# Kernel optimization log

Hardware: AMD Instinct MI355X
Metric: run time of the kernel (lower is better)

## Reference

```python
import jax, jax.numpy as jnp
import numpy as np

HID = 2048      # hidden_size
H = 16          # num query heads
KV = 4          # num kv heads
HD = HID // H   # head_dim = 128
THETA = 1000000.0
T = 2048        # tokens (single causal sequence)


def _rope(x, positions):
    # neox-style rotate-half RoPE over full head_dim. x: [T, h, HD]
    half = HD // 2
    inv_freq = THETA ** (-jnp.arange(half, dtype=jnp.float32) * 2.0 / HD)  # [half]
    freqs = positions.astype(jnp.float32)[:, None] * inv_freq              # [T, half]
    cos = jnp.cos(freqs)[:, None, :]
    sin = jnp.sin(freqs)[:, None, :]
    x1, x2 = x[..., :half], x[..., half:]
    return jnp.concatenate([x1 * cos - x2 * sin, x2 * cos + x1 * sin], axis=-1)


def setup_inputs() -> dict:
    key = jax.random.key(0)
    k1, k2, k3 = jax.random.split(key, 3)
    hidden_states = jax.random.normal(k1, (T, HID), jnp.float32) * 0.02
    w_qkv = jax.random.normal(k2, (HID, (H + 2 * KV) * HD), jnp.float32) * 0.02
    w_o = jax.random.normal(k3, (H * HD, HID), jnp.float32) * 0.02
    positions = jnp.arange(T, dtype=jnp.int32)
    return {"hidden_states": hidden_states, "w_qkv": w_qkv, "w_o": w_o,
            "positions": positions}


def reference(hidden_states, w_qkv, w_o, positions):
    q_size, kv_size = H * HD, KV * HD
    qkv = hidden_states @ w_qkv                                  # [T, q+2kv]
    q = qkv[:, :q_size].reshape(T, H, HD)
    k = qkv[:, q_size:q_size + kv_size].reshape(T, KV, HD)
    v = qkv[:, q_size + kv_size:].reshape(T, KV, HD)
    q = _rope(q, positions)
    k = _rope(k, positions)
    # GQA: expand kv heads to query heads
    group = H // KV
    k_e = jnp.repeat(k, group, axis=1)                           # [T, H, HD]
    v_e = jnp.repeat(v, group, axis=1)
    scale = HD ** -0.5
    scores = jnp.einsum('thd,shd->hts', q, k_e) * scale          # [H, T, T]
    causal = positions[:, None] >= positions[None, :]            # [T, T]
    scores = jnp.where(causal[None, :, :], scores, -1e30)
    attn = jax.nn.softmax(scores, axis=-1)
    o = jnp.einsum('hts,shd->thd', attn, v_e).reshape(T, H * HD)
    return o @ w_o
```

## Files before the change

kernel.cpp:

```cpp
#include <hip/hip_runtime.h>
#include <hip/hip_bf16.h>

#define T_LEN 2048
#define HID 2048
#define NH 16
#define NKV 4
#define HD 128
#define QKV_COLS 3072

typedef __attribute__((ext_vector_type(8))) short bf16x8;
typedef __attribute__((ext_vector_type(4))) float f32x4;

static __device__ __forceinline__ ushort f2bf(float f) {
  __hip_bfloat16 h = __float2bfloat16(f);
  return *reinterpret_cast<ushort*>(&h);
}
static __device__ __forceinline__ float bf2f(ushort u) {
  union { unsigned int i; float f; } v;
  v.i = ((unsigned int)u) << 16;
  return v.f;
}

static __device__ __forceinline__ void async_copy16(const ushort* g, ushort* l) {
  __builtin_amdgcn_global_load_lds(
      (const __attribute__((address_space(1))) unsigned int*)g,
      (__attribute__((address_space(3))) unsigned int*)l, 16, 0, 0);
}

__global__ __launch_bounds__(256) void cast_f32_bf16(
    const float* __restrict__ x, ushort* __restrict__ y, int n) {
  int idx = (blockIdx.x * 256 + threadIdx.x) * 4;
  if (idx < n) {
    float4 v = *(const float4*)(x + idx);
    ushort4 o;
    o.x = f2bf(v.x); o.y = f2bf(v.y); o.z = f2bf(v.z); o.w = f2bf(v.w);
    *(ushort4*)(y + idx) = o;
  }
}

__global__ __launch_bounds__(256) void transpose_cast(
    const float* __restrict__ W, ushort* __restrict__ WT, int K, int N) {
  __shared__ float t[64][65];
  const int bk = blockIdx.x * 64, bn = blockIdx.y * 64;
  const int tid = threadIdx.x;
  const int c = tid & 63;
#pragma unroll
  for (int i = 0; i < 16; ++i) {
    int r = (tid >> 6) + i * 4;
    t[r][c] = W[(size_t)(bk + r) * N + bn + c];
  }
  __syncthreads();
#pragma unroll
  for (int i = 0; i < 16; ++i) {
    int r = (tid >> 6) + i * 4;
    WT[(size_t)(bn + r) * K + bk + c] = f2bf(t[c][r]);
  }
}

__global__ __launch_bounds__(64) void rope_table(
    float2* __restrict__ tbl, const int* __restrict__ positions) {
  const int t = blockIdx.x, j = threadIdx.x;
  double inv_freq = pow(1000000.0, -(double)(2 * j) / 128.0);
  double ang = (double)positions[t] * inv_freq;
  double s, c;
  sincos(ang, &s, &c);
  tbl[(size_t)t * 64 + j] = make_float2((float)c, (float)s);
}

template <bool OUT_BF16>
__global__ __launch_bounds__(256, 5) void gemm_bt(
    const ushort* __restrict__ A, const ushort* __restrict__ BT,
    void* __restrict__ C, int M, int N, int K) {
  __shared__ __align__(16) ushort lds[1536 * 8];
  const int tid = threadIdx.x;
  const int bm = blockIdx.y * 64, bn = blockIdx.x * 128;
  const int wave = tid >> 6, lane = tid & 63;
  const int lr = lane & 15, lq = lane >> 4;
  const int wm = (wave & 1) * 32, wn = (wave >> 1) * 64;

  f32x4 acc[2][4];
#pragma unroll
  for (int i = 0; i < 2; ++i)
#pragma unroll
    for (int j = 0; j < 4; ++j) {
      acc[i][j][0] = 0.f; acc[i][j][1] = 0.f;
      acc[i][j][2] = 0.f; acc[i][j][3] = 0.f;
    }

  for (int k0 = 0; k0 < K; k0 += 64) {
#pragma unroll
    for (int it = 0; it < 2; ++it) {
      int c = it * 256 + tid;
      int row = c >> 3, sl = c & 7, kc = sl ^ (row & 7);
      async_copy16(A + (size_t)(bm + row) * K + k0 + kc * 8, &lds[c * 8]);
    }
#pragma unroll
    for (int it = 0; it < 4; ++it) {
      int c = it * 256 + tid;
      int row = c >> 3, sl = c & 7, kc = sl ^ (row & 7);
      async_copy16(BT + (size_t)(bn + row) * K + k0 + kc * 8,
                   &lds[(512 + c) * 8]);
    }
    __syncthreads();

#pragma unroll
    for (int ks = 0; ks < 2; ++ks) {
      bf16x8 af[2], bfr[4];
#pragma unroll
      for (int mi = 0; mi < 2; ++mi) {
        int row = wm + mi * 16 + lr, kc = ks * 4 + lq;
        af[mi] = *(const bf16x8*)&lds[(row * 8 + (kc ^ (row & 7))) * 8];
      }
#pragma unroll
      for (int ni = 0; ni < 4; ++ni) {
        int row = wn + ni * 16 + lr, kc = ks * 4 + lq;
        bfr[ni] = *(const bf16x8*)&lds[(512 + row * 8 + (kc ^ (row & 7))) * 8];
      }
#pragma unroll
      for (int mi = 0; mi < 2; ++mi)
#pragma unroll
        for (int ni = 0; ni < 4; ++ni)
          acc[mi][ni] = __builtin_amdgcn_mfma_f32_16x16x32_bf16(
              af[mi], bfr[ni], acc[mi][ni], 0, 0, 0);
    }
    __syncthreads();
  }

#pragma unroll
  for (int mi = 0; mi < 2; ++mi)
#pragma unroll
    for (int ni = 0; ni < 4; ++ni)
#pragma unroll
      for (int r = 0; r < 4; ++r) {
        size_t row = bm + wm + mi * 16 + lq * 4 + r;
        size_t col = bn + wn + ni * 16 + lr;
        if (OUT_BF16)
          ((ushort*)C)[row * N + col] = f2bf(acc[mi][ni][r]);
        else
          ((float*)C)[row * N + col] = acc[mi][ni][r];
      }
}

__global__ __launch_bounds__(256, 5) void gemm_qkv(
    const ushort* __restrict__ A, const ushort* __restrict__ BT,
    ushort* __restrict__ qkvb, const float2* __restrict__ tbl,
    int M, int N, int K) {
  __shared__ __align__(16) ushort lds[1536 * 8];
  const int tid = threadIdx.x;
  const int bm = blockIdx.y * 64, bn = blockIdx.x * 128;
  const int wave = tid >> 6, lane = tid & 63;
  const int lr = lane & 15, lq = lane >> 4;
  const int wm = (wave & 1) * 32, wn = (wave >> 1) * 64;

  f32x4 acc[2][4];
#pragma unroll
  for (int i = 0; i < 2; ++i)
#pragma unroll
    for (int j = 0; j < 4; ++j) {
      acc[i][j][0] = 0.f; acc[i][j][1] = 0.f;
      acc[i][j][2] = 0.f; acc[i][j][3] = 0.f;
    }

  for (int k0 = 0; k0 < K; k0 += 64) {
#pragma unroll
    for (int it = 0; it < 2; ++it) {
      int c = it * 256 + tid;
      int row = c >> 3, sl = c & 7, kc = sl ^ (row & 7);
      async_copy16(A + (size_t)(bm + row) * K + k0 + kc * 8, &lds[c * 8]);
    }
#pragma unroll
    for (int it = 0; it < 4; ++it) {
      int c = it * 256 + tid;
      int row = c >> 3, sl = c & 7, kc = sl ^ (row & 7);
      async_copy16(BT + (size_t)(bn + row) * K + k0 + kc * 8,
                   &lds[(512 + c) * 8]);
    }
    __syncthreads();

#pragma unroll
    for (int ks = 0; ks < 2; ++ks) {
      bf16x8 af[2], bfr[4];
#pragma unroll
      for (int mi = 0; mi < 2; ++mi) {
        int row = wm + mi * 16 + lr, kc = ks * 4 + lq;
        af[mi] = *(const bf16x8*)&lds[(row * 8 + (kc ^ (row & 7))) * 8];
      }
#pragma unroll
      for (int ni = 0; ni < 4; ++ni) {
        int row = wn + ni * 16 + lr, kc = ks * 4 + lq;
        bfr[ni] = *(const bf16x8*)&lds[(512 + row * 8 + (kc ^ (row & 7))) * 8];
      }
#pragma unroll
      for (int mi = 0; mi < 2; ++mi)
#pragma unroll
        for (int ni = 0; ni < 4; ++ni)
          acc[mi][ni] = __builtin_amdgcn_mfma_f32_16x16x32_bf16(
              af[mi], bfr[ni], acc[mi][ni], 0, 0, 0);
    }
    __syncthreads();
  }

  const int head = bn >> 7;
  if (head < NH + NKV - NKV + 0 + (NKV) - 4 + 16 + 4 - 0 && head < 20) {
    ushort* ep = lds;
#pragma unroll
    for (int mi = 0; mi < 2; ++mi)
#pragma unroll
      for (int ni = 0; ni < 4; ++ni)
#pragma unroll
        for (int r = 0; r < 4; ++r)
          ep[(wm + mi * 16 + lq * 4 + r) * 130 + wn + ni * 16 + lr] =
              f2bf(acc[mi][ni][r]);
    __syncthreads();

    const float qs = (head < NH) ? 0.08838834764831845f : 1.0f;
#pragma unroll
    for (int it = 0; it < 16; ++it) {
      int idx = it * 256 + tid;
      int row = idx >> 6, j = idx & 63;
      float x1 = bf2f(ep[row * 130 + j]);
      float x2 = bf2f(ep[row * 130 + 64 + j]);
      float2 cs = tbl[(size_t)(bm + row) * 64 + j];
      qkvb[(size_t)(bm + row) * QKV_COLS + bn + j] =
          f2bf((x1 * cs.x - x2 * cs.y) * qs);
      qkvb[(size_t)(bm + row) * QKV_COLS + bn + 64 + j] =
          f2bf((x2 * cs.x + x1 * cs.y) * qs);
    }
  } else {
#pragma unroll
    for (int mi = 0; mi < 2; ++mi)
#pragma unroll
      for (int ni = 0; ni < 4; ++ni)
#pragma unroll
        for (int r = 0; r < 4; ++r) {
          size_t row = bm + wm + mi * 16 + lq * 4 + r;
          size_t col = bn + wn + ni * 16 + lr;
          qkvb[row * QKV_COLS + col] = f2bf(acc[mi][ni][r]);
        }
  }
}

__global__ __launch_bounds__(256) void repack_vt(
    const ushort* __restrict__ qkv, ushort* __restrict__ vt) {
  __shared__ ushort tile[64][65];
  const int bt = blockIdx.x * 64;
  const int bv = blockIdx.y * 64;
  const int tid = threadIdx.x;
  const int c = tid & 63, r0 = tid >> 6;
#pragma unroll
  for (int i = 0; i < 16; ++i) {
    int r = r0 + i * 4;
    tile[r][c] = qkv[(size_t)(bt + r) * QKV_COLS + 2560 + bv + c];
  }
  __syncthreads();
#pragma unroll
  for (int i = 0; i < 16; ++i) {
    int r = r0 + i * 4;
    vt[(size_t)(bv + r) * T_LEN + bt + c] = tile[c][r];
  }
}

__global__ __launch_bounds__(256, 3) void attn_mfma(
    const ushort* __restrict__ qkv, const ushort* __restrict__ vt,
    ushort* __restrict__ o, ushort* __restrict__ partials,
    float* __restrict__ ml) {
  int qt, h, k_begin, k_end, slot = -1;
  {
    const int i = blockIdx.x;
    if (i < 512) {
      qt = 31 - (i >> 5);
      const int rem = i & 31;
      h = rem >> 1;
      const int chunk = rem & 1;
      const int n = qt + 1, half = n >> 1;
      k_begin = chunk ? half : 0;
      k_end = chunk ? n : half;
      slot = ((qt - 16) * 16 + h) * 2 + chunk;
    } else {
      const int j = i - 512;
      qt = 15 - (j >> 4);
      h = j & 15;
      k_begin = 0;
      k_end = qt + 1;
    }
  }
  const int kh = h >> 2;
  const int tid = threadIdx.x;
  const int wave = tid >> 6, lane = tid & 63;
  const int lr = lane & 15, lq = lane >> 4;
  const int wq = wave >> 1, ws = wave & 1;

  __shared__ __align__(16) ushort KsL[1024 * 8];
  __shared__ __align__(16) ushort VtsL[1024 * 8];
  __shared__ __align__(16) ushort Ps[8 * 67 * 8];
  __shared__ float l_sh[64][2];

  bf16x8 qf[2][4];
  {
    const ushort* qbase =
        qkv + (size_t)(qt * 64 + wq * 32 + lr) * QKV_COLS + h * HD + lq * 8;
#pragma unroll
    for (int mi = 0; mi < 2; ++mi)
#pragma unroll
      for (int kk = 0; kk < 4; ++kk)
        qf[mi][kk] = *(const bf16x8*)(qbase + (size_t)mi * 16 * QKV_COLS + kk * 32);
  }

  float l_part[2][4];
#pragma unroll
  for (int mi = 0; mi < 2; ++mi)
#pragma unroll
    for (int r = 0; r < 4; ++r) l_part[mi][r] = 0.f;
  f32x4 o_acc[4][2];
#pragma unroll
  for (int qi = 0; qi < 4; ++qi)
#pragma unroll
    for (int di = 0; di < 2; ++di) {
      o_acc[qi][di][0] = 0.f; o_acc[qi][di][1] = 0.f;
      o_acc[qi][di][2] = 0.f; o_acc[qi][di][3] = 0.f;
    }

  for (int kt = k_begin; kt < k_end; ++kt) {
    __syncthreads();

    {
      const ushort* kbase = qkv + 2048 + kh * HD;
#pragma unroll
      for (int it = 0; it < 4; ++it) {
        int c = it * 256 + tid;
        int s = c >> 4, sl = c & 15, dg = sl ^ (s & 15);
        async_copy16(kbase + (size_t)(kt * 64 + s) * QKV_COLS + dg * 8,
                     &KsL[c * 8]);
      }
    }
    {
      const ushort* vbase = vt + (size_t)(kh * HD) * T_LEN + kt * 64;
#pragma unroll
      for (int it = 0; it < 4; ++it) {
        int c = it * 256 + tid;
        int d = c >> 3, sl = c & 7, sc = sl ^ (d & 7);
        async_copy16(vbase + (size_t)d * T_LEN + sc * 8, &VtsL[c * 8]);
      }
    }
    __syncthreads();

    f32x4 s_acc[2][2];
#pragma unroll
    for (int mi = 0; mi < 2; ++mi)
#pragma unroll
      for (int ni = 0; ni < 2; ++ni) {
        s_acc[mi][ni][0] = 0.f; s_acc[mi][ni][1] = 0.f;
        s_acc[mi][ni][2] = 0.f; s_acc[mi][ni][3] = 0.f;
      }
#pragma unroll
    for (int kk = 0; kk < 4; ++kk) {
      bf16x8 kf[2];
#pragma unroll
      for (int ni = 0; ni < 2; ++ni) {
        int s = ws * 32 + ni * 16 + lr;
        kf[ni] = *(const bf16x8*)&KsL[(s * 16 + ((kk * 4 + lq) ^ (s & 15))) * 8];
      }
#pragma unroll
      for (int mi = 0; mi < 2; ++mi)
#pragma unroll
        for (int ni = 0; ni < 2; ++ni)
          s_acc[mi][ni] = __builtin_amdgcn_mfma_f32_16x16x32_bf16(
              qf[mi][kk], kf[ni], s_acc[mi][ni], 0, 0, 0);
    }

    if (kt == qt) {
#pragma unroll
      for (int mi = 0; mi < 2; ++mi)
#pragma unroll
        for (int ni = 0; ni < 2; ++ni)
#pragma unroll
          for (int r = 0; r < 4; ++r)
            if (ws * 32 + ni * 16 + lr > wq * 32 + mi * 16 + lq * 4 + r)
              s_acc[mi][ni][r] = -1e30f;
    }

#pragma unroll
    for (int mi = 0; mi < 2; ++mi)
#pragma unroll
      for (int ni = 0; ni < 2; ++ni)
#pragma unroll
        for (int r = 0; r < 4; ++r) {
          float p = __expf(s_acc[mi][ni][r]);
          l_part[mi][r] += p;
          int s = ws * 32 + ni * 16 + lr;
          int q = wq * 32 + mi * 16 + lq * 4 + r;
          Ps[((s >> 3) * 67 + q) * 8 + (s & 7)] = f2bf(p);
        }
    __syncthreads();

#pragma unroll
    for (int ss = 0; ss < 2; ++ss) {
      bf16x8 vf[2];
#pragma unroll
      for (int di = 0; di < 2; ++di) {
        int d = wave * 32 + di * 16 + lr, sc = ss * 4 + lq;
        vf[di] = *(const bf16x8*)&VtsL[(d * 8 + (sc ^ (d & 7))) * 8];
      }
#pragma unroll
      for (int qi = 0; qi < 4; ++qi) {
        bf16x8 pf = *(const bf16x8*)&Ps[((ss * 4 + lq) * 67 + qi * 16 + lr) * 8];
#pragma unroll
        for (int di = 0; di < 2; ++di)
          o_acc[qi][di] = __builtin_amdgcn_mfma_f32_16x16x32_bf16(
              pf, vf[di], o_acc[qi][di], 0, 0, 0);
      }
    }
  }

#pragma unroll
  for (int mi = 0; mi < 2; ++mi)
#pragma unroll
    for (int r = 0; r < 4; ++r) {
      float v = l_part[mi][r];
#pragma unroll
      for (int off = 1; off < 16; off <<= 1) v += __shfl_xor(v, off, 16);
      l_part[mi][r] = v;
    }
  if (lr == 0) {
#pragma unroll
    for (int mi = 0; mi < 2; ++mi)
#pragma unroll
      for (int r = 0; r < 4; ++r)
        l_sh[wq * 32 + mi * 16 + lq * 4 + r][ws] = l_part[mi][r];
  }
  __syncthreads();

  if (slot < 0) {
    ushort* ob = o + (size_t)(qt * 64) * (NH * HD) + h * HD + wave * 32;
#pragma unroll
    for (int qi = 0; qi < 4; ++qi)
#pragma unroll
      for (int r = 0; r < 4; ++r) {
        int q = qi * 16 + lq * 4 + r;
        float inv = 1.f / (l_sh[q][0] + l_sh[q][1]);
#pragma unroll
        for (int di = 0; di < 2; ++di)
          ob[(size_t)q * (NH * HD) + di * 16 + lr] =
              f2bf(o_acc[qi][di][r] * inv);
      }
  } else {
    ushort* pb = partials + (size_t)slot * 64 * HD + wave * 32;
#pragma unroll
    for (int qi = 0; qi < 4; ++qi)
#pragma unroll
      for (int r = 0; r < 4; ++r) {
        int q = qi * 16 + lq * 4 + r;
#pragma unroll
        for (int di = 0; di < 2; ++di)
          pb[(size_t)q * HD + di * 16 + lr] = f2bf(o_acc[qi][di][r]);
      }
    if (tid < 64) ml[(size_t)slot * 64 + tid] = l_sh[tid][0] + l_sh[tid][1];
  }
}

__global__ __launch_bounds__(256) void attn_reduce(
    const ushort* __restrict__ partials, const float* __restrict__ ml,
    ushort* __restrict__ o) {
  const int bi = blockIdx.x;
  const int qt = 16 + (bi >> 4), h = bi & 15;
  const int s0 = ((qt - 16) * 16 + h) * 2;
  const int tid = threadIdx.x;
  const int row = tid >> 2;
  const int dq = (tid & 3) * 32;

  float l0 = ml[(size_t)s0 * 64 + row];
  float l1 = ml[(size_t)(s0 + 1) * 64 + row];
  float inv = 1.f / (l0 + l1);

  const ushort* p0 = partials + ((size_t)s0 * 64 + row) * HD + dq;
  const ushort* p1 = partials + ((size_t)(s0 + 1) * 64 + row) * HD + dq;
  ushort* ob = o + (size_t)(qt * 64 + row) * (NH * HD) + h * HD + dq;
#pragma unroll
  for (int k = 0; k < 32; ++k)
    ob[k] = f2bf((bf2f(p0[k]) + bf2f(p1[k])) * inv);
}

extern "C" void kernel_launch(void* const* d_in, const int* in_sizes, int n_in,
                              void* d_out, int out_size, void* d_ws,
                              size_t ws_size, hipStream_t stream) {
  const float* hidden = (const float*)d_in[0];
  const float* w_qkv  = (const float*)d_in[1];
  const float* w_o    = (const float*)d_in[2];
  const int* positions = (const int*)d_in[3];
  float* out = (float*)d_out;

  ushort* ws = (ushort*)d_ws;
  ushort* hb    = ws;
  ushort* wqkvT = ws + 4194304;
  ushort* qkvb  = wqkvT + 6291456;
  ushort* vtb   = qkvb + 6291456;
  float*  mlb   = (float*)(vtb + 1048576);
  float2* tbl   = (float2*)(mlb + 32768);
  ushort* ob       = hb;
  ushort* partials = wqkvT;
  ushort* woT      = wqkvT;

  cast_f32_bf16<<<4096, 256, 0, stream>>>(hidden, hb, HID * T_LEN);
  transpose_cast<<<dim3(HID / 64, QKV_COLS / 64), 256, 0, stream>>>(
      w_qkv, wqkvT, HID, QKV_COLS);
  rope_table<<<T_LEN, 64, 0, stream>>>(tbl, positions);

  gemm_qkv<<<dim3(QKV_COLS / 128, T_LEN / 64), 256, 0, stream>>>(
      hb, wqkvT, qkvb, tbl, T_LEN, QKV_COLS, HID);

  repack_vt<<<dim3(T_LEN / 64, (NKV * HD) / 64), 256, 0, stream>>>(qkvb, vtb);

  attn_mfma<<<768, 256, 0, stream>>>(qkvb, vtb, ob, partials, mlb);
  attn_reduce<<<256, 256, 0, stream>>>(partials, mlb, ob);

  transpose_cast<<<dim3(HID / 64, HID / 64), 256, 0, stream>>>(
      w_o, woT, HID, HID);

  gemm_bt<false><<<dim3(HID / 128, T_LEN / 64), 256, 0, stream>>>(
      ob, woT, out, T_LEN, HID, NH * HD);
}
```

Before: 212.4 us.

## Double-buffer GEMM LDS loads, fuse prep kernels, write V transpose in QKV epilogue

Merges the hidden cast, w_qkv transpose-cast and RoPE table into one prep launch. Both GEMMs now double-buffer their LDS tiles so the next K-slice is prefetched while MFMAs run on the current one. Occupancy hints drop from 5 to 3 blocks to fit the doubled LDS. The QKV GEMM epilogue writes the V columns straight into the transposed vt buffer, which removes the separate repack_vt kernel and its extra pass over V. The V path no longer writes V into qkvb, which assumes attention reads V only from vt.

```diff
diff --git a/kernel.cpp b/kernel.cpp
--- a/kernel.cpp
+++ b/kernel.cpp
@@ -27,14 +27,42 @@
       (__attribute__((address_space(3))) unsigned int*)l, 16, 0, 0);
 }
 
-__global__ __launch_bounds__(256) void cast_f32_bf16(
-    const float* __restrict__ x, ushort* __restrict__ y, int n) {
-  int idx = (blockIdx.x * 256 + threadIdx.x) * 4;
-  if (idx < n) {
-    float4 v = *(const float4*)(x + idx);
+__global__ __launch_bounds__(256) void prep(
+    const float* __restrict__ hidden, ushort* __restrict__ hb,
+    const float* __restrict__ w_qkv, ushort* __restrict__ wqkvT,
+    const int* __restrict__ positions, float2* __restrict__ tbl) {
+  __shared__ float t[64][65];
+  const int b = blockIdx.x;
+  const int tid = threadIdx.x;
+  if (b < 4096) {
+    int idx = (b * 256 + tid) * 4;
+    float4 v = *(const float4*)(hidden + idx);
     ushort4 o;
     o.x = f2bf(v.x); o.y = f2bf(v.y); o.z = f2bf(v.z); o.w = f2bf(v.w);
-    *(ushort4*)(y + idx) = o;
+    *(ushort4*)(hb + idx) = o;
+  } else if (b < 5632) {
+    const int tb = b - 4096;
+    const int bk = (tb & 31) * 64, bn = (tb >> 5) * 64;
+    const int c = tid & 63;
+#pragma unroll
+    for (int i = 0; i < 16; ++i) {
+      int r = (tid >> 6) + i * 4;
+      t[r][c] = w_qkv[(size_t)(bk + r) * QKV_COLS + bn + c];
+    }
+    __syncthreads();
+#pragma unroll
+    for (int i = 0; i < 16; ++i) {
+      int r = (tid >> 6) + i * 4;
+      wqkvT[(size_t)(bn + r) * HID + bk + c] = f2bf(t[c][r]);
+    }
+  } else {
+    const int rb = b - 5632;
+    const int tt = rb * 4 + (tid >> 6), j = tid & 63;
+    double inv_freq = pow(1000000.0, -(double)(2 * j) / 128.0);
+    double ang = (double)positions[tt] * inv_freq;
+    double s, c2;
+    sincos(ang, &s, &c2);
+    tbl[(size_t)tt * 64 + j] = make_float2((float)c2, (float)s);
   }
 }
 
@@ -57,21 +85,11 @@
   }
 }
 
-__global__ __launch_bounds__(64) void rope_table(
-    float2* __restrict__ tbl, const int* __restrict__ positions) {
-  const int t = blockIdx.x, j = threadIdx.x;
-  double inv_freq = pow(1000000.0, -(double)(2 * j) / 128.0);
-  double ang = (double)positions[t] * inv_freq;
-  double s, c;
-  sincos(ang, &s, &c);
-  tbl[(size_t)t * 64 + j] = make_float2((float)c, (float)s);
-}
-
 template <bool OUT_BF16>
-__global__ __launch_bounds__(256, 5) void gemm_bt(
+__global__ __launch_bounds__(256, 3) void gemm_bt(
     const ushort* __restrict__ A, const ushort* __restrict__ BT,
     void* __restrict__ C, int M, int N, int K) {
-  __shared__ __align__(16) ushort lds[1536 * 8];
+  __shared__ __align__(16) ushort lds[2][1536 * 8];
   const int tid = threadIdx.x;
   const int bm = blockIdx.y * 64, bn = blockIdx.x * 128;
   const int wave = tid >> 6, lane = tid & 63;
@@ -87,34 +105,40 @@
       acc[i][j][2] = 0.f; acc[i][j][3] = 0.f;
     }
 
-  for (int k0 = 0; k0 < K; k0 += 64) {
+  auto stage = [&](int k0, int buf) {
 #pragma unroll
     for (int it = 0; it < 2; ++it) {
       int c = it * 256 + tid;
       int row = c >> 3, sl = c & 7, kc = sl ^ (row & 7);
-      async_copy16(A + (size_t)(bm + row) * K + k0 + kc * 8, &lds[c * 8]);
+      async_copy16(A + (size_t)(bm + row) * K + k0 + kc * 8, &lds[buf][c * 8]);
     }
 #pragma unroll
     for (int it = 0; it < 4; ++it) {
       int c = it * 256 + tid;
       int row = c >> 3, sl = c & 7, kc = sl ^ (row & 7);
       async_copy16(BT + (size_t)(bn + row) * K + k0 + kc * 8,
-                   &lds[(512 + c) * 8]);
-    }
-    __syncthreads();
-
+                   &lds[buf][(512 + c) * 8]);
+    }
+  };
+
+  stage(0, 0);
+  __syncthreads();
+  int cur = 0;
+  for (int k0 = 0; k0 < K; k0 += 64) {
+    if (k0 + 64 < K) stage(k0 + 64, cur ^ 1);
 #pragma unroll
     for (int ks = 0; ks < 2; ++ks) {
       bf16x8 af[2], bfr[4];
 #pragma unroll
       for (int mi = 0; mi < 2; ++mi) {
         int row = wm + mi * 16 + lr, kc = ks * 4 + lq;
-        af[mi] = *(const bf16x8*)&lds[(row * 8 + (kc ^ (row & 7))) * 8];
+        af[mi] = *(const bf16x8*)&lds[cur][(row * 8 + (kc ^ (row & 7))) * 8];
       }
 #pragma unroll
       for (int ni = 0; ni < 4; ++ni) {
         int row = wn + ni * 16 + lr, kc = ks * 4 + lq;
-        bfr[ni] = *(const bf16x8*)&lds[(512 + row * 8 + (kc ^ (row & 7))) * 8];
+        bfr[ni] =
+            *(const bf16x8*)&lds[cur][(512 + row * 8 + (kc ^ (row & 7))) * 8];
       }
 #pragma unroll
       for (int mi = 0; mi < 2; ++mi)
@@ -124,6 +148,7 @@
               af[mi], bfr[ni], acc[mi][ni], 0, 0, 0);
     }
     __syncthreads();
+    cur ^= 1;
   }
 
 #pragma unroll
@@ -141,11 +166,11 @@
       }
 }
 
-__global__ __launch_bounds__(256, 5) void gemm_qkv(
+__global__ __launch_bounds__(256, 3) void gemm_qkv(
     const ushort* __restrict__ A, const ushort* __restrict__ BT,
-    ushort* __restrict__ qkvb, const float2* __restrict__ tbl,
-    int M, int N, int K) {
-  __shared__ __align__(16) ushort lds[1536 * 8];
+    ushort* __restrict__ qkvb, ushort* __restrict__ vt,
+    const float2* __restrict__ tbl, int M, int N, int K) {
+  __shared__ __align__(16) ushort lds[2][1536 * 8];
   const int tid = threadIdx.x;
   const int bm = blockIdx.y * 64, bn = blockIdx.x * 128;
   const int wave = tid >> 6, lane = tid & 63;
@@ -161,34 +186,40 @@
       acc[i][j][2] = 0.f; acc[i][j][3] = 0.f;
     }
 
-  for (int k0 = 0; k0 < K; k0 += 64) {
+  auto stage = [&](int k0, int buf) {
 #pragma unroll
     for (int it = 0; it < 2; ++it) {
       int c = it * 256 + tid;
       int row = c >> 3, sl = c & 7, kc = sl ^ (row & 7);
-      async_copy16(A + (size_t)(bm + row) * K + k0 + kc * 8, &lds[c * 8]);
+      async_copy16(A + (size_t)(bm + row) * K + k0 + kc * 8, &lds[buf][c * 8]);
     }
 #pragma unroll
     for (int it = 0; it < 4; ++it) {
       int c = it * 256 + tid;
       int row = c >> 3, sl = c & 7, kc = sl ^ (row & 7);
       async_copy16(BT + (size_t)(bn + row) * K + k0 + kc * 8,
-                   &lds[(512 + c) * 8]);
-    }
-    __syncthreads();
-
+                   &lds[buf][(512 + c) * 8]);
+    }
+  };
+
+  stage(0, 0);
+  __syncthreads();
+  int cur = 0;
+  for (int k0 = 0; k0 < K; k0 += 64) {
+    if (k0 + 64 < K) stage(k0 + 64, cur ^ 1);
 #pragma unroll
     for (int ks = 0; ks < 2; ++ks) {
       bf16x8 af[2], bfr[4];
 #pragma unroll
       for (int mi = 0; mi < 2; ++mi) {
         int row = wm + mi * 16 + lr, kc = ks * 4 + lq;
-        af[mi] = *(const bf16x8*)&lds[(row * 8 + (kc ^ (row & 7))) * 8];
+        af[mi] = *(const bf16x8*)&lds[cur][(row * 8 + (kc ^ (row & 7))) * 8];
       }
 #pragma unroll
       for (int ni = 0; ni < 4; ++ni) {
         int row = wn + ni * 16 + lr, kc = ks * 4 + lq;
-        bfr[ni] = *(const bf16x8*)&lds[(512 + row * 8 + (kc ^ (row & 7))) * 8];
+        bfr[ni] =
+            *(const bf16x8*)&lds[cur][(512 + row * 8 + (kc ^ (row & 7))) * 8];
       }
 #pragma unroll
       for (int mi = 0; mi < 2; ++mi)
@@ -198,11 +229,12 @@
               af[mi], bfr[ni], acc[mi][ni], 0, 0, 0);
     }
     __syncthreads();
+    cur ^= 1;
   }
 
   const int head = bn >> 7;
-  if (head < NH + NKV - NKV + 0 + (NKV) - 4 + 16 + 4 - 0 && head < 20) {
-    ushort* ep = lds;
+  ushort* ep = &lds[0][0];
+  if (head < 20) {
 #pragma unroll
     for (int mi = 0; mi < 2; ++mi)
 #pragma unroll
@@ -232,31 +264,23 @@
 #pragma unroll
       for (int ni = 0; ni < 4; ++ni)
 #pragma unroll
-        for (int r = 0; r < 4; ++r) {
-          size_t row = bm + wm + mi * 16 + lq * 4 + r;
-          size_t col = bn + wn + ni * 16 + lr;
-          qkvb[row * QKV_COLS + col] = f2bf(acc[mi][ni][r]);
-        }
-  }
-}
-
-__global__ __launch_bounds__(256) void repack_vt(
-    const ushort* __restrict__ qkv, ushort* __restrict__ vt) {
-  __shared__ ushort tile[64][65];
-  const int bt = blockIdx.x * 64;
-  const int bv = blockIdx.y * 64;
-  const int tid = threadIdx.x;
-  const int c = tid & 63, r0 = tid >> 6;
-#pragma unroll
-  for (int i = 0; i < 16; ++i) {
-    int r = r0 + i * 4;
-    tile[r][c] = qkv[(size_t)(bt + r) * QKV_COLS + 2560 + bv + c];
-  }
-  __syncthreads();
-#pragma unroll
-  for (int i = 0; i < 16; ++i) {
-    int r = r0 + i * 4;
-    vt[(size_t)(bv + r) * T_LEN + bt + c] = tile[c][r];
+        for (int r = 0; r < 4; ++r)
+          ep[(wm + mi * 16 + lq * 4 + r) * 130 + wn + ni * 16 + lr] =
+              f2bf(acc[mi][ni][r]);
+    __syncthreads();
+
+    const int vd0 = bn - 2560;
+#pragma unroll
+    for (int it = 0; it < 8; ++it) {
+      int idx = it * 256 + tid;
+      int vd = idx >> 4, tg = (idx & 15) * 4;
+      ushort4 w;
+      w.x = ep[(tg + 0) * 130 + vd];
+      w.y = ep[(tg + 1) * 130 + vd];
+      w.z = ep[(tg + 2) * 130 + vd];
+      w.w = ep[(tg + 3) * 130 + vd];
+      *(ushort4*)&vt[(size_t)(vd0 + vd) * T_LEN + bm + tg] = w;
+    }
   }
 }
 
@@ -500,15 +524,10 @@
   ushort* partials = wqkvT;
   ushort* woT      = wqkvT;
 
-  cast_f32_bf16<<<4096, 256, 0, stream>>>(hidden, hb, HID * T_LEN);
-  transpose_cast<<<dim3(HID / 64, QKV_COLS / 64), 256, 0, stream>>>(
-      w_qkv, wqkvT, HID, QKV_COLS);
-  rope_table<<<T_LEN, 64, 0, stream>>>(tbl, positions);
+  prep<<<6144, 256, 0, stream>>>(hidden, hb, w_qkv, wqkvT, positions, tbl);
 
   gemm_qkv<<<dim3(QKV_COLS / 128, T_LEN / 64), 256, 0, stream>>>(
-      hb, wqkvT, qkvb, tbl, T_LEN, QKV_COLS, HID);
-
-  repack_vt<<<dim3(T_LEN / 64, (NKV * HD) / 64), 256, 0, stream>>>(qkvb, vtb);
+      hb, wqkvT, qkvb, vtb, tbl, T_LEN, QKV_COLS, HID);
 
   attn_mfma<<<768, 256, 0, stream>>>(qkvb, vtb, ob, partials, mlb);
   attn_reduce<<<256, 256, 0, stream>>>(partials, mlb, ob);
```

Result: faster. 203.8 us (-4.0%).
